# Kernel optimization log

Hardware: AMD Instinct MI355X
Metric: run time of the kernel (lower is better)

Reference implementation:

```python
import jax, jax.numpy as jnp
import numpy as np

D_Q = D_K = D_V = 1024
H = 16
D_ATT = 64
NQ = NK = 4096
EPS = 1e-12


def setup_inputs() -> dict:
    key = jax.random.key(0)
    ks = jax.random.split(key, 12)
    s_in = 1.0 / np.sqrt(D_Q)
    s_out = 1.0 / np.sqrt(H * D_ATT)
    return {
        "queries": jax.random.normal(ks[0], (NQ, D_Q), jnp.float32),
        "keys": jax.random.normal(ks[1], (NK, D_K), jnp.float32),
        "values": jax.random.normal(ks[2], (NK, D_V), jnp.float32),
        "Wq": jax.random.uniform(ks[3], (D_Q, H * D_ATT), jnp.float32, -s_in, s_in),
        "bq": jax.random.uniform(ks[4], (H * D_ATT,), jnp.float32, -s_in, s_in),
        "Wk": jax.random.uniform(ks[5], (D_K, H * D_ATT), jnp.float32, -s_in, s_in),
        "bk": jax.random.uniform(ks[6], (H * D_ATT,), jnp.float32, -s_in, s_in),
        "Wv": jax.random.uniform(ks[7], (D_V, H * D_ATT), jnp.float32, -s_in, s_in),
        "bv": jax.random.uniform(ks[8], (H * D_ATT,), jnp.float32, -s_in, s_in),
        "Wo": jax.random.uniform(ks[9], (H * D_ATT, D_Q), jnp.float32, -s_out, s_out),
        "bo": jax.random.uniform(ks[10], (D_Q,), jnp.float32, -s_out, s_out),
        "gamma": jnp.ones((D_Q,), jnp.float32),
        "beta": jnp.zeros((D_Q,), jnp.float32),
    }


def reference(queries, keys, values, Wq, bq, Wk, bk, Wv, bv, Wo, bo, gamma, beta):
    nq = queries.shape[0]
    nk = keys.shape[0]
    # projections -> (n, h, d)
    q = (queries @ Wq + bq).reshape(nq, H, D_ATT)
    k = (keys @ Wk + bk).reshape(nk, H, D_ATT)
    v = (values @ Wv + bv).reshape(nk, H, D_ATT)
    # scores (h, nq, nk)
    att = jnp.einsum("qhd,khd->hqk", q, k) / np.sqrt(D_ATT).astype(np.float32)
    att = jax.nn.softmax(att, axis=-1)  # dropout = identity (eval)
    out = jnp.einsum("hqk,khd->qhd", att, v).reshape(nq, H * D_ATT)
    out = queries + out @ Wo + bo
    # LayerNorm, eps=1e-12
    mu = jnp.mean(out, axis=-1, keepdims=True)
    var = jnp.mean(jnp.square(out - mu), axis=-1, keepdims=True)
    out = (out - mu) * jax.lax.rsqrt(var + EPS) * gamma + beta
    return out
```

## Files before the change

kernel.cpp:

```cpp
#include <hip/hip_runtime.h>
#include <stdint.h>

typedef unsigned short u16;
typedef unsigned int u32;
typedef __attribute__((ext_vector_type(8))) __bf16 bf16x8;
typedef __attribute__((ext_vector_type(2))) __bf16 bf16x2;
typedef __attribute__((ext_vector_type(4))) float f32x4;
typedef __attribute__((ext_vector_type(16))) float f32x16;
typedef __attribute__((ext_vector_type(8))) u16 u16x8;
typedef __attribute__((ext_vector_type(4))) u32 u32x4;

#define Q_SCALE 0.1803368801111204f

__device__ __forceinline__ float ex2(float x) { return __builtin_amdgcn_exp2f(x); }

__device__ __forceinline__ u16 f2bf(float f) {
  __bf16 h = (__bf16)f;
  return __builtin_bit_cast(u16, h);
}
__device__ __forceinline__ float bf2f(u16 u) {
  u32 x = ((u32)u) << 16;
  return __builtin_bit_cast(float, x);
}
__device__ __forceinline__ u32 pack2(float a, float b) {
  bf16x2 v; v.x = (__bf16)a; v.y = (__bf16)b;
  return __builtin_bit_cast(u32, v);
}
__device__ __forceinline__ void gl_lds16(const void* g, void* l) {
  __builtin_amdgcn_global_load_lds((const __attribute__((address_space(1))) void*)g,
                                   (__attribute__((address_space(3))) void*)l, 16, 0, 0);
}

__global__ __launch_bounds__(256) void prep_kernel(const float* __restrict__ q,
                                                   const float* __restrict__ k,
                                                   const float* __restrict__ v,
                                                   u16* __restrict__ xdst,
                                                   const float* __restrict__ Wq,
                                                   const float* __restrict__ Wk,
                                                   const float* __restrict__ Wv,
                                                   const float* __restrict__ Wo,
                                                   u16* __restrict__ wcatT,
                                                   u16* __restrict__ woT) {
  __shared__ u16 tile[64][72];
  int z = blockIdx.z;
  int t = threadIdx.x;
  if (z == 4) {
    int b = blockIdx.y * 16 + blockIdx.x;
#pragma unroll 4
    for (int it = 0; it < 24; ++it) {
      size_t tt = (size_t)b * 6144 + it * 256 + t;
      size_t e = tt * 8;
      int which = (int)(e >> 22);
      const float* s = which == 0 ? q : which == 1 ? k : v;
      size_t off = e & 4194303;
      float4 a = *(const float4*)(s + off);
      float4 bb = *(const float4*)(s + off + 4);
      u16x8 o;
      o[0] = f2bf(a.x); o[1] = f2bf(a.y); o[2] = f2bf(a.z); o[3] = f2bf(a.w);
      o[4] = f2bf(bb.x); o[5] = f2bf(bb.y); o[6] = f2bf(bb.z); o[7] = f2bf(bb.w);
      *(u16x8*)(xdst + e) = o;
    }
    return;
  }
  const float* W = z == 0 ? Wq : z == 1 ? Wk : z == 2 ? Wv : Wo;
  int k0 = blockIdx.y * 64, n0 = blockIdx.x * 64;
  int r = t >> 2, c0 = (t & 3) * 16;
  const float* src = W + (size_t)(k0 + r) * 1024 + n0 + c0;
#pragma unroll
  for (int i = 0; i < 16; i += 4) {
    float4 x = *(const float4*)(src + i);
    tile[r][c0 + i] = f2bf(x.x); tile[r][c0 + i + 1] = f2bf(x.y);
    tile[r][c0 + i + 2] = f2bf(x.z); tile[r][c0 + i + 3] = f2bf(x.w);
  }
  __syncthreads();
  int n = t >> 2, kc = (t & 3) * 16;
  u16x8 o0, o1;
#pragma unroll
  for (int j = 0; j < 8; ++j) { o0[j] = tile[kc + j][n]; o1[j] = tile[kc + 8 + j][n]; }
  u16* dst = (z < 3) ? (wcatT + (size_t)z * 1048576 + (size_t)(n0 + n) * 1024 + k0 + kc)
                     : (woT + (size_t)(n0 + n) * 1024 + k0 + kc);
  *(u16x8*)dst = o0;
  *(u16x8*)(dst + 8) = o1;
}

__global__ __launch_bounds__(256) void gemm_bt(const u16* __restrict__ A,
                                               const u16* __restrict__ BT,
                                               u16* __restrict__ outBF,
                                               float* __restrict__ outF,
                                               const float* __restrict__ b0,
                                               const float* __restrict__ b1,
                                               const float* __restrict__ b2,
                                               const float* __restrict__ resid,
                                               int mode) {
  __shared__ u16 As[2][4096];
  __shared__ u16 Bs[2][4096];
  int tid = threadIdx.x;
  int bid = blockIdx.y * 8 + blockIdx.x;
  int cpx = (gridDim.y * 8) >> 3;
  int swz = (bid & 7) * cpx + (bid >> 3);
  int m0 = (swz >> 3) * 128, n0 = (swz & 7) * 128;
  const u16* bt = (mode == 0) ? (BT + (size_t)(m0 >> 12) * 1048576) : BT;
  int w = tid >> 6, l = tid & 63;
  int wr = w >> 1, wc = w & 1;
  f32x4 acc[4][4];
#pragma unroll
  for (int i = 0; i < 4; ++i)
#pragma unroll
    for (int j = 0; j < 4; ++j)
#pragma unroll
      for (int rr = 0; rr < 4; ++rr) acc[i][j][rr] = 0.f;

  auto stage = [&](int buf, int kt) {
#pragma unroll
    for (int i = 0; i < 2; ++i) {
      int id = i * 256 + tid;
      int r = id >> 2, cp = id & 3;
      int cl = cp ^ ((r ^ (r >> 2)) & 3);
      gl_lds16(A + (size_t)(m0 + r) * 1024 + kt * 32 + cl * 8, &As[buf][id * 8]);
      gl_lds16(bt + (size_t)(n0 + r) * 1024 + kt * 32 + cl * 8, &Bs[buf][id * 8]);
    }
  };
  stage(0, 0);
  __syncthreads();
  int sw = (l & 3) ^ ((l >> 2) & 3);
  int phys = (l >> 4) ^ sw;
  for (int kt = 0; kt < 32; ++kt) {
    int buf = kt & 1;
    if (kt < 31) stage(buf ^ 1, kt + 1);
    bf16x8 af[4], bfr[4];
#pragma unroll
    for (int mi = 0; mi < 4; ++mi) {
      int row = wr * 64 + mi * 16 + (l & 15);
      af[mi] = *(const bf16x8*)&As[buf][row * 32 + phys * 8];
    }
#pragma unroll
    for (int nj = 0; nj < 4; ++nj) {
      int rowb = wc * 64 + nj * 16 + (l & 15);
      bfr[nj] = *(const bf16x8*)&Bs[buf][rowb * 32 + phys * 8];
    }
#pragma unroll
    for (int mi = 0; mi < 4; ++mi)
#pragma unroll
      for (int nj = 0; nj < 4; ++nj)
        acc[mi][nj] = __builtin_amdgcn_mfma_f32_16x16x32_bf16(af[mi], bfr[nj],
                                                              acc[mi][nj], 0, 0, 0);
    __syncthreads();
  }
#pragma unroll
  for (int mi = 0; mi < 4; ++mi)
#pragma unroll
    for (int nj = 0; nj < 4; ++nj)
#pragma unroll
      for (int rr = 0; rr < 4; ++rr) {
        int row = m0 + wr * 64 + mi * 16 + (l >> 4) * 4 + rr;
        int col = n0 + wc * 64 + nj * 16 + (l & 15);
        float vv = acc[mi][nj][rr];
        if (mode == 0) {
          int sec = row >> 12, orow = row & 4095;
          const float* bp = sec == 0 ? b0 : sec == 1 ? b1 : b2;
          vv += bp[col];
          if (sec == 0) vv *= Q_SCALE;
          outBF[(size_t)sec * 4194304 + (size_t)orow * 1024 + col] = f2bf(vv);
        } else {
          vv += b0[col] + resid[(size_t)row * 1024 + col];
          outF[(size_t)row * 1024 + col] = vv;
        }
      }
}

__global__ __launch_bounds__(256) void vtrans_kernel(const u16* __restrict__ vp,
                                                     u16* __restrict__ vt) {
  __shared__ u16 tile[64][72];
  int t = threadIdx.x;
  int n0 = blockIdx.x * 64, h = blockIdx.y;
  int r = t >> 2, c0 = (t & 3) * 16;
  u16x8 a = *(const u16x8*)(vp + (size_t)(n0 + r) * 1024 + h * 64 + c0);
  u16x8 b = *(const u16x8*)(vp + (size_t)(n0 + r) * 1024 + h * 64 + c0 + 8);
#pragma unroll
  for (int j = 0; j < 8; ++j) { tile[r][c0 + j] = a[j]; tile[r][c0 + 8 + j] = b[j]; }
  __syncthreads();
  int d = t >> 2, nc = (t & 3) * 16;
  u16x8 o0, o1;
#pragma unroll
  for (int j = 0; j < 8; ++j) { o0[j] = tile[nc + j][d]; o1[j] = tile[nc + 8 + j][d]; }
  size_t base = (size_t)(h * 64 + d) * 4096 + n0 + nc;
  *(u16x8*)(vt + base) = o0;
  *(u16x8*)(vt + base + 8) = o1;
}

__global__ __launch_bounds__(512, 4) void attn_kernel(const u16* __restrict__ qp,
                                                      const u16* __restrict__ kp,
                                                      const u16* __restrict__ vt,
                                                      u16* __restrict__ attout) {
  __shared__ u16 smem[32768];
  int tid = threadIdx.x;
  int w = tid >> 6, l = tid & 63;
  int half = w >> 2, wl = w & 3;
  int hi = l >> 5, l31 = l & 31, l7 = l & 7;
  int h = blockIdx.y, bx = blockIdx.x;
  int qrow = bx * 128 + wl * 32 + l31;
  bf16x8 qf[4];
#pragma unroll
  for (int ds = 0; ds < 4; ++ds)
    qf[ds] = *(const bf16x8*)(qp + (size_t)qrow * 1024 + h * 64 + ds * 16 + hi * 8);

  f32x16 zero16;
#pragma unroll
  for (int r = 0; r < 16; ++r) zero16[r] = 0.f;
  f32x16 accO[2];
#pragma unroll
  for (int r = 0; r < 16; ++r) { accO[0][r] = 0.f; accO[1][r] = 0.f; }
  float l_run = 0.f;

  u16* sbase = smem + half * 16384;
  int ht = (wl << 6) | l;
  const u16* srcK[2]; const u16* srcV[2]; int dstOff[2];
#pragma unroll
  for (int i = 0; i < 2; ++i) {
    int id = i * 256 + ht;
    int r = id >> 3, cp = id & 7, cl = cp ^ (r & 7);
    srcK[i] = kp + (size_t)(half * 2048 + r) * 1024 + h * 64 + cl * 8;
    srcV[i] = vt + (size_t)(h * 64 + r) * 4096 + half * 2048 + cl * 8;
    dstOff[i] = id * 8;
  }
  auto stage = [&](int buf, int kt) {
    u16* b = sbase + buf * 8192;
#pragma unroll
    for (int i = 0; i < 2; ++i) {
      gl_lds16(srcK[i] + (size_t)kt * 65536, b + dstOff[i]);
      gl_lds16(srcV[i] + kt * 64, b + 4096 + dstOff[i]);
    }
  };
  stage(0, 0);
  __syncthreads();

  for (int kt = 0; kt < 32; ++kt) {
    int buf = kt & 1;
    if (kt < 31) stage(buf ^ 1, kt + 1);
    const u16* Kt = sbase + buf * 8192;
    const u16* Vt = Kt + 4096;

    f32x16 accS[2];
    __builtin_amdgcn_s_setprio(1);
#pragma unroll
    for (int mt = 0; mt < 2; ++mt) {
      int row = mt * 32 + l31;
      {
        bf16x8 kf = *(const bf16x8*)(Kt + row * 64 + ((0 + hi) ^ l7) * 8);
        accS[mt] = __builtin_amdgcn_mfma_f32_32x32x16_bf16(kf, qf[0], zero16, 0, 0, 0);
      }
#pragma unroll
      for (int ds = 1; ds < 4; ++ds) {
        int phys = (2 * ds + hi) ^ l7;
        bf16x8 kf = *(const bf16x8*)(Kt + row * 64 + phys * 8);
        accS[mt] = __builtin_amdgcn_mfma_f32_32x32x16_bf16(kf, qf[ds], accS[mt], 0, 0, 0);
      }
    }
    __builtin_amdgcn_s_setprio(0);

    u32 pku[2][8];
    float s0 = 0.f, s1 = 0.f, s2 = 0.f, s3 = 0.f;
#pragma unroll
    for (int mt = 0; mt < 2; ++mt)
#pragma unroll
      for (int qd = 0; qd < 8; ++qd) {
        float a = ex2(accS[mt][2 * qd]);
        float b = ex2(accS[mt][2 * qd + 1]);
        if (qd & 1) { s2 += a; s3 += b; } else { s0 += a; s1 += b; }
        pku[mt][qd] = pack2(a, b);
      }
    float t1 = (s0 + s1) + (s2 + s3);
    t1 += __shfl_xor(t1, 32, 64);
    l_run += t1;

    bf16x8 pb[4];
#pragma unroll
    for (int ks = 0; ks < 4; ++ks) {
      const int mt = ks >> 1, k1 = ks & 1;
      u32 a0 = pku[mt][4 * k1 + 0], c0 = pku[mt][4 * k1 + 2];
      u32 a1 = pku[mt][4 * k1 + 1], c1 = pku[mt][4 * k1 + 3];
      asm("v_permlane32_swap_b32 %0, %1" : "+v"(a0), "+v"(c0));
      asm("v_permlane32_swap_b32 %0, %1" : "+v"(a1), "+v"(c1));
      u32x4 fr;
      fr[0] = a0; fr[1] = a1; fr[2] = c0; fr[3] = c1;
      pb[ks] = __builtin_bit_cast(bf16x8, fr);
    }
    __builtin_amdgcn_s_setprio(1);
#pragma unroll
    for (int mto = 0; mto < 2; ++mto) {
      int row = mto * 32 + l31;
#pragma unroll
      for (int ks = 0; ks < 4; ++ks) {
        int phys = (2 * ks + hi) ^ l7;
        bf16x8 vf = *(const bf16x8*)(Vt + row * 64 + phys * 8);
        accO[mto] = __builtin_amdgcn_mfma_f32_32x32x16_bf16(vf, pb[ks], accO[mto], 0, 0, 0);
      }
    }
    __builtin_amdgcn_s_setprio(0);
    __syncthreads();
  }

  u16* pO = smem;
  float* ml = (float*)(smem + 2 * 128 * 72);
  int q = wl * 32 + l31;
#pragma unroll
  for (int mto = 0; mto < 2; ++mto)
#pragma unroll
    for (int g = 0; g < 4; ++g)
#pragma unroll
      for (int j = 0; j < 2; ++j) {
        int r = g * 4 + j * 2;
        int d = j * 2 + 8 * g + 4 * hi + 32 * mto;
        u32 pk = pack2(accO[mto][r], accO[mto][r + 1]);
        *(u32*)&pO[(size_t)(half * 128 + q) * 72 + d] = pk;
      }
  if (hi == 0) ml[half * 128 + q] = l_run;
  __syncthreads();
  {
    int qq = tid >> 2, d0 = (tid & 3) * 16;
    float invL = 1.f / (ml[qq] + ml[128 + qq]);
    u16x8 ra0 = *(u16x8*)&pO[(size_t)qq * 72 + d0];
    u16x8 ra1 = *(u16x8*)&pO[(size_t)qq * 72 + d0 + 8];
    u16x8 rb0 = *(u16x8*)&pO[(size_t)(128 + qq) * 72 + d0];
    u16x8 rb1 = *(u16x8*)&pO[(size_t)(128 + qq) * 72 + d0 + 8];
    u16x8 o0, o1;
#pragma unroll
    for (int j = 0; j < 8; ++j) {
      o0[j] = f2bf((bf2f(ra0[j]) + bf2f(rb0[j])) * invL);
      o1[j] = f2bf((bf2f(ra1[j]) + bf2f(rb1[j])) * invL);
    }
    size_t ob = (size_t)(bx * 128 + qq) * 1024 + (size_t)h * 64 + d0;
    *(u16x8*)(attout + ob) = o0;
    *(u16x8*)(attout + ob + 8) = o1;
  }
}

__global__ __launch_bounds__(256) void ln_kernel(float* __restrict__ io,
                                                 const float* __restrict__ gamma,
                                                 const float* __restrict__ beta) {
  int row = blockIdx.x, t = threadIdx.x;
  float4 v = *(const float4*)(io + (size_t)row * 1024 + t * 4);
  float s = v.x + v.y + v.z + v.w;
  float sq = v.x * v.x + v.y * v.y + v.z * v.z + v.w * v.w;
#pragma unroll
  for (int off = 1; off < 64; off <<= 1) {
    s += __shfl_xor(s, off, 64);
    sq += __shfl_xor(sq, off, 64);
  }
  __shared__ float rs[4], rq[4];
  if ((t & 63) == 0) { rs[t >> 6] = s; rq[t >> 6] = sq; }
  __syncthreads();
  float S = rs[0] + rs[1] + rs[2] + rs[3];
  float Q = rq[0] + rq[1] + rq[2] + rq[3];
  float mu = S * (1.f / 1024.f);
  float var = Q * (1.f / 1024.f) - mu * mu;
  float invs = rsqrtf(var + 1e-12f);
  float4 g = *(const float4*)(gamma + t * 4);
  float4 b = *(const float4*)(beta + t * 4);
  float4 o;
  o.x = (v.x - mu) * invs * g.x + b.x;
  o.y = (v.y - mu) * invs * g.y + b.y;
  o.z = (v.z - mu) * invs * g.z + b.z;
  o.w = (v.w - mu) * invs * g.w + b.w;
  *(float4*)(io + (size_t)row * 1024 + t * 4) = o;
}

extern "C" void kernel_launch(void* const* d_in, const int* in_sizes, int n_in,
                              void* d_out, int out_size, void* d_ws, size_t ws_size,
                              hipStream_t stream) {
  (void)in_sizes; (void)n_in; (void)out_size; (void)ws_size;
  const float* queries = (const float*)d_in[0];
  const float* keys    = (const float*)d_in[1];
  const float* values  = (const float*)d_in[2];
  const float* Wq = (const float*)d_in[3];
  const float* bq = (const float*)d_in[4];
  const float* Wk = (const float*)d_in[5];
  const float* bk = (const float*)d_in[6];
  const float* Wv = (const float*)d_in[7];
  const float* bv = (const float*)d_in[8];
  const float* Wo = (const float*)d_in[9];
  const float* bo = (const float*)d_in[10];
  const float* gamma = (const float*)d_in[11];
  const float* beta  = (const float*)d_in[12];
  float* out = (float*)d_out;

  u16* ws = (u16*)d_ws;
  u16* xq     = ws;
  u16* attout = ws;
  u16* vt     = ws + 4194304;
  u16* wcatT  = ws + 12582912;
  u16* woT    = ws + 15728640;
  u16* qp     = ws + 16777216;
  u16* kp     = qp + 4194304;
  u16* vp     = qp + 8388608;

  prep_kernel<<<dim3(16, 16, 5), dim3(256), 0, stream>>>(queries, keys, values, xq,
                                                         Wq, Wk, Wv, Wo, wcatT, woT);
  gemm_bt<<<dim3(8, 96), dim3(256), 0, stream>>>(xq, wcatT, qp, nullptr,
                                                 bq, bk, bv, nullptr, 0);
  vtrans_kernel<<<dim3(64, 16), dim3(256), 0, stream>>>(vp, vt);
  attn_kernel<<<dim3(32, 16), dim3(512), 0, stream>>>(qp, kp, vt, attout);
  gemm_bt<<<dim3(8, 32), dim3(256), 0, stream>>>(attout, woT, nullptr, out,
                                                 bo, nullptr, nullptr, queries, 1);
  ln_kernel<<<dim3(4096), dim3(256), 0, stream>>>(out, gamma, beta);
}
```

Baseline: 196.4 us.

## Split output GEMM into 128x64 tile kernel and fix attention LDS swizzle

The output projection GEMM moves to a dedicated kernel with 128x64 tiles, which doubles the block count from 256 to 512 so the GPU's compute units are better filled for the 4096x1024 output. The QKV GEMM is specialised to drop its mode branch. Separately, the attention kernel's K/V shared-memory swizzle now XORs in higher row bits, aiming to cut LDS bank conflicts. In exchange, the smaller tiles reuse less data per block and load A from global more often.

```diff
diff --git a/kernel.cpp b/kernel.cpp
--- a/kernel.cpp
+++ b/kernel.cpp
@@ -86,20 +86,17 @@
 __global__ __launch_bounds__(256) void gemm_bt(const u16* __restrict__ A,
                                                const u16* __restrict__ BT,
                                                u16* __restrict__ outBF,
-                                               float* __restrict__ outF,
                                                const float* __restrict__ b0,
                                                const float* __restrict__ b1,
-                                               const float* __restrict__ b2,
-                                               const float* __restrict__ resid,
-                                               int mode) {
+                                               const float* __restrict__ b2) {
   __shared__ u16 As[2][4096];
   __shared__ u16 Bs[2][4096];
   int tid = threadIdx.x;
   int bid = blockIdx.y * 8 + blockIdx.x;
-  int cpx = (gridDim.y * 8) >> 3;
+  int cpx = gridDim.y;
   int swz = (bid & 7) * cpx + (bid >> 3);
   int m0 = (swz >> 3) * 128, n0 = (swz & 7) * 128;
-  const u16* bt = (mode == 0) ? (BT + (size_t)(m0 >> 12) * 1048576) : BT;
+  const u16* bt = BT + (size_t)(m0 >> 12) * 1048576;
   int w = tid >> 6, l = tid & 63;
   int wr = w >> 1, wc = w & 1;
   f32x4 acc[4][4];
@@ -155,16 +152,86 @@
         int row = m0 + wr * 64 + mi * 16 + (l >> 4) * 4 + rr;
         int col = n0 + wc * 64 + nj * 16 + (l & 15);
         float vv = acc[mi][nj][rr];
-        if (mode == 0) {
-          int sec = row >> 12, orow = row & 4095;
-          const float* bp = sec == 0 ? b0 : sec == 1 ? b1 : b2;
-          vv += bp[col];
-          if (sec == 0) vv *= Q_SCALE;
-          outBF[(size_t)sec * 4194304 + (size_t)orow * 1024 + col] = f2bf(vv);
-        } else {
-          vv += b0[col] + resid[(size_t)row * 1024 + col];
-          outF[(size_t)row * 1024 + col] = vv;
-        }
+        int sec = row >> 12, orow = row & 4095;
+        const float* bp = sec == 0 ? b0 : sec == 1 ? b1 : b2;
+        vv += bp[col];
+        if (sec == 0) vv *= Q_SCALE;
+        outBF[(size_t)sec * 4194304 + (size_t)orow * 1024 + col] = f2bf(vv);
+      }
+}
+
+__global__ __launch_bounds__(256) void gemm_n64(const u16* __restrict__ A,
+                                                const u16* __restrict__ BT,
+                                                float* __restrict__ outF,
+                                                const float* __restrict__ b0,
+                                                const float* __restrict__ resid) {
+  __shared__ u16 As[2][4096];
+  __shared__ u16 Bs[2][2048];
+  int tid = threadIdx.x;
+  int bid = blockIdx.y * 8 + blockIdx.x;
+  int swz = (bid & 7) * 64 + (bid >> 3);
+  int m0 = (swz >> 4) * 128, n0 = (swz & 15) * 64;
+  int w = tid >> 6, l = tid & 63;
+  int wr = w >> 1, wc = w & 1;
+  f32x4 acc[4][2];
+#pragma unroll
+  for (int i = 0; i < 4; ++i)
+#pragma unroll
+    for (int j = 0; j < 2; ++j)
+#pragma unroll
+      for (int rr = 0; rr < 4; ++rr) acc[i][j][rr] = 0.f;
+
+  auto stage = [&](int buf, int kt) {
+#pragma unroll
+    for (int i = 0; i < 2; ++i) {
+      int id = i * 256 + tid;
+      int r = id >> 2, cp = id & 3;
+      int cl = cp ^ ((r ^ (r >> 2)) & 3);
+      gl_lds16(A + (size_t)(m0 + r) * 1024 + kt * 32 + cl * 8, &As[buf][id * 8]);
+    }
+    {
+      int id = tid;
+      int r = id >> 2, cp = id & 3;
+      int cl = cp ^ ((r ^ (r >> 2)) & 3);
+      gl_lds16(BT + (size_t)(n0 + r) * 1024 + kt * 32 + cl * 8, &Bs[buf][id * 8]);
+    }
+  };
+  stage(0, 0);
+  __syncthreads();
+  int sw = (l & 3) ^ ((l >> 2) & 3);
+  int phys = (l >> 4) ^ sw;
+  for (int kt = 0; kt < 32; ++kt) {
+    int buf = kt & 1;
+    if (kt < 31) stage(buf ^ 1, kt + 1);
+    bf16x8 af[4], bfr[2];
+#pragma unroll
+    for (int mi = 0; mi < 4; ++mi) {
+      int row = wr * 64 + mi * 16 + (l & 15);
+      af[mi] = *(const bf16x8*)&As[buf][row * 32 + phys * 8];
+    }
+#pragma unroll
+    for (int nj = 0; nj < 2; ++nj) {
+      int rowb = wc * 32 + nj * 16 + (l & 15);
+      bfr[nj] = *(const bf16x8*)&Bs[buf][rowb * 32 + phys * 8];
+    }
+#pragma unroll
+    for (int mi = 0; mi < 4; ++mi)
+#pragma unroll
+      for (int nj = 0; nj < 2; ++nj)
+        acc[mi][nj] = __builtin_amdgcn_mfma_f32_16x16x32_bf16(af[mi], bfr[nj],
+                                                              acc[mi][nj], 0, 0, 0);
+    __syncthreads();
+  }
+#pragma unroll
+  for (int mi = 0; mi < 4; ++mi)
+#pragma unroll
+    for (int nj = 0; nj < 2; ++nj)
+#pragma unroll
+      for (int rr = 0; rr < 4; ++rr) {
+        int row = m0 + wr * 64 + mi * 16 + (l >> 4) * 4 + rr;
+        int col = n0 + wc * 32 + nj * 16 + (l & 15);
+        outF[(size_t)row * 1024 + col] =
+            acc[mi][nj][rr] + b0[col] + resid[(size_t)row * 1024 + col];
       }
 }
 
@@ -218,7 +285,8 @@
 #pragma unroll
   for (int i = 0; i < 2; ++i) {
     int id = i * 256 + ht;
-    int r = id >> 3, cp = id & 7, cl = cp ^ (r & 7);
+    int r = id >> 3, cp = id & 7;
+    int cl = cp ^ ((r ^ (r >> 3)) & 7);
     srcK[i] = kp + (size_t)(half * 2048 + r) * 1024 + h * 64 + cl * 8;
     srcV[i] = vt + (size_t)(h * 64 + r) * 4096 + half * 2048 + cl * 8;
     dstOff[i] = id * 8;
@@ -245,13 +313,14 @@
 #pragma unroll
     for (int mt = 0; mt < 2; ++mt) {
       int row = mt * 32 + l31;
+      int g = (row ^ (row >> 3)) & 7;
       {
-        bf16x8 kf = *(const bf16x8*)(Kt + row * 64 + ((0 + hi) ^ l7) * 8);
+        bf16x8 kf = *(const bf16x8*)(Kt + row * 64 + ((0 + hi) ^ g) * 8);
         accS[mt] = __builtin_amdgcn_mfma_f32_32x32x16_bf16(kf, qf[0], zero16, 0, 0, 0);
       }
 #pragma unroll
       for (int ds = 1; ds < 4; ++ds) {
-        int phys = (2 * ds + hi) ^ l7;
+        int phys = (2 * ds + hi) ^ g;
         bf16x8 kf = *(const bf16x8*)(Kt + row * 64 + phys * 8);
         accS[mt] = __builtin_amdgcn_mfma_f32_32x32x16_bf16(kf, qf[ds], accS[mt], 0, 0, 0);
       }
@@ -289,9 +358,10 @@
 #pragma unroll
     for (int mto = 0; mto < 2; ++mto) {
       int row = mto * 32 + l31;
+      int g = (row ^ (row >> 3)) & 7;
 #pragma unroll
       for (int ks = 0; ks < 4; ++ks) {
-        int phys = (2 * ks + hi) ^ l7;
+        int phys = (2 * ks + hi) ^ g;
         bf16x8 vf = *(const bf16x8*)(Vt + row * 64 + phys * 8);
         accO[mto] = __builtin_amdgcn_mfma_f32_32x32x16_bf16(vf, pb[ks], accO[mto], 0, 0, 0);
       }
@@ -396,11 +466,9 @@
 
   prep_kernel<<<dim3(16, 16, 5), dim3(256), 0, stream>>>(queries, keys, values, xq,
                                                          Wq, Wk, Wv, Wo, wcatT, woT);
-  gemm_bt<<<dim3(8, 96), dim3(256), 0, stream>>>(xq, wcatT, qp, nullptr,
-                                                 bq, bk, bv, nullptr, 0);
+  gemm_bt<<<dim3(8, 96), dim3(256), 0, stream>>>(xq, wcatT, qp, bq, bk, bv);
   vtrans_kernel<<<dim3(64, 16), dim3(256), 0, stream>>>(vp, vt);
   attn_kernel<<<dim3(32, 16), dim3(512), 0, stream>>>(qp, kp, vt, attout);
-  gemm_bt<<<dim3(8, 32), dim3(256), 0, stream>>>(attout, woT, nullptr, out,
-                                                 bo, nullptr, nullptr, queries, 1);
+  gemm_n64<<<dim3(8, 64), dim3(256), 0, stream>>>(attout, woT, out, bo, queries);
   ln_kernel<<<dim3(4096), dim3(256), 0, stream>>>(out, gamma, beta);
 }
```

Result: faster. 174.5 us (-11.2%).
